# Optimization experiments

Measured on AMD Instinct MI355X. Metric: run time of the kernel, lower is better.

The kernel has to match this reference:

```python
import jax, jax.numpy as jnp
import numpy as np

K = 1048576          # number of shooting particles (k); x also has K points
LR = 0.25            # fixed-point gradient-descent learning rate
N_ITERS = 20         # nr_of_fixed_point_iterations
nl = jnp.tanh        # nonlinearity='tanh'


def _advect(z, t1, b1, t2, b2):
    # z: [n, 2, 1]; t*: [2,2]; b*: [2,1]. dot z = theta1 @ nl(theta2 @ z + b2) + b1
    return jnp.matmul(t1, nl(jnp.matmul(t2, z) + b2)) + b1


def _lagrangian(t1, b1, t2, b2, q, p, invK, invKb):
    eye = jnp.eye(2, dtype=t1.dtype)
    v1 = t1.reshape(-1)
    v2 = (t2 - eye).reshape(-1)
    kinetic = 0.5 * (v1 @ invK @ v1 + v2 @ invK @ v2
                     + b1[:, 0] @ invKb @ b1[:, 0] + b2[:, 0] @ invKb @ b2[:, 0])
    potential = jnp.mean(p * _advect(q, t1, b1, t2, b2))
    return kinetic - potential


def _run_fixed_point(q, p, t1, b1, t2, b2, invK, invKb):
    grad_fn = jax.grad(_lagrangian, argnums=(0, 1, 2, 3))
    def step(carry, _):
        t1, b1, t2, b2 = carry
        g1, gb1, g2, gb2 = grad_fn(t1, b1, t2, b2, q, p, invK, invKb)
        return (t1 - LR * g1, b1 - LR * gb1, t2 - LR * g2, b2 - LR * gb2), None
    carry, _ = jax.lax.scan(step, (t1, b1, t2, b2), None, length=N_ITERS)
    return carry


def setup_inputs() -> dict:
    key = jax.random.key(0)
    k1, k2, k3, k4, k5 = jax.random.split(key, 5)
    inp = jax.random.normal(k1, (3 * K, 1, 2), dtype=jnp.float32)
    return {
        "t": jnp.zeros((1,), dtype=jnp.float32),
        "inp": inp,
        "theta1_init": jax.random.normal(k2, (2, 2), dtype=jnp.float32),
        "bias1_init": jax.random.normal(k3, (2, 1), dtype=jnp.float32),
        "theta2_init": jax.random.normal(k4, (2, 2), dtype=jnp.float32),
        "bias2_init": jax.random.normal(k5, (2, 1), dtype=jnp.float32),
        "inv_Kbar": jnp.eye(4, dtype=jnp.float32),    # Kbar = I(d^2) -> inverse = I
        "inv_Kbar_b": jnp.eye(2, dtype=jnp.float32),  # Kbar_b = I(d) -> inverse = I
        "k": K,
    }


def reference(t, inp, theta1_init, bias1_init, theta2_init, bias2_init,
              inv_Kbar, inv_Kbar_b, k):
    qt, pt, xt = inp[:k], inp[k:2 * k], inp[2 * k:]
    q = jnp.swapaxes(qt, 1, 2)  # [k, 2, 1]
    p = jnp.swapaxes(pt, 1, 2)
    x = jnp.swapaxes(xt, 1, 2)

    def final_thetas(qv):
        return _run_fixed_point(qv, p, theta1_init, bias1_init,
                                theta2_init, bias2_init, inv_Kbar, inv_Kbar_b)

    t1, b1, t2, b2 = final_thetas(q)

    # dot_p = dL/dq of the final Lagrangian, including dependence of the
    # fixed-point thetas on q (torch uses create_graph=True throughout).
    def L_of_q(qv):
        ft1, fb1, ft2, fb2 = final_thetas(qv)
        return _lagrangian(ft1, fb1, ft2, fb2, qv, p, inv_Kbar, inv_Kbar_b)

    dot_p = jax.grad(L_of_q)(q)
    dot_x = _advect(x, t1, b1, t2, b2)
    dot_q = _advect(q, t1, b1, t2, b2)

    return jnp.concatenate([jnp.swapaxes(dot_q, 1, 2),
                            jnp.swapaxes(dot_p, 1, 2),
                            jnp.swapaxes(dot_x, 1, 2)], axis=0)
```

## Files before the change

kernel.cpp:

```cpp
#include <hip/hip_runtime.h>


#define LR 0.25f
#define NIT 20
#define TPB 512
#define NB  256
#define GUARD (1<<18)

typedef float v2f __attribute__((ext_vector_type(2)));
typedef unsigned long long u64;

__device__ __forceinline__ u64 ld64_ag(const u64* p){
    return __hip_atomic_load(p, __ATOMIC_RELAXED, __HIP_MEMORY_SCOPE_AGENT);
}
__device__ __forceinline__ void st64_ep(u64* p, float v, unsigned ep){
    u64 x = ((u64)ep << 32) | (u64)__float_as_uint(v);
    __hip_atomic_store(p, x, __ATOMIC_RELAXED, __HIP_MEMORY_SCOPE_AGENT);
}
__device__ __forceinline__ unsigned ep_of(u64 x){ return (unsigned)(x >> 32); }
__device__ __forceinline__ float    val_of(u64 x){ return __uint_as_float((unsigned)(x & 0xffffffffull)); }

__device__ __forceinline__ v2f tanh2(v2f x){
    v2f e;
    e.x = __expf(x.x + x.x);
    e.y = __expf(x.y + x.y);
    v2f d = e + 1.0f;
    v2f r;
    r.x = __builtin_amdgcn_rcpf(d.x);
    r.y = __builtin_amdgcn_rcpf(d.y);
    return 1.0f - (r + r);
}

#define DPP_ADD(x, ctrl) ((x) + __int_as_float(__builtin_amdgcn_update_dpp(0, __float_as_int(x), (ctrl), 0xF, 0xF, true)))
__device__ __forceinline__ float wave_sum64(float x){
    x = DPP_ADD(x, 0x111);
    x = DPP_ADD(x, 0x112);
    x = DPP_ADD(x, 0x114);
    x = DPP_ADD(x, 0x118);
    x = DPP_ADD(x, 0x142);
    x = DPP_ADD(x, 0x143);
    return x;
}

__device__ __forceinline__ void compute_grad(const float* s, const float* th,
                                             const float* ksym, const float* ksymb,
                                             float c, float* g){
    const float Ivec[4]={1.f,0.f,0.f,1.f};
    #pragma unroll
    for(int j=0;j<4;j++){
        float kv=0.f;
        #pragma unroll
        for(int m=0;m<4;m++) kv += ksym[j*4+m]*th[m];
        g[j] = kv - c*s[j];
    }
    #pragma unroll
    for(int i2=0;i2<2;i2++)
        g[4+i2] = ksymb[i2*2+0]*th[4] + ksymb[i2*2+1]*th[5] - c*s[4+i2];
    #pragma unroll
    for(int j=0;j<4;j++){
        float kv=0.f;
        #pragma unroll
        for(int m=0;m<4;m++) kv += ksym[j*4+m]*(th[6+m]-Ivec[m]);
        g[6+j] = kv - c*s[6+j];
    }
    #pragma unroll
    for(int i2=0;i2<2;i2++)
        g[10+i2] = ksymb[i2*2+0]*th[10] + ksymb[i2*2+1]*th[11] - c*s[10+i2];
}

__device__ __forceinline__ void accum_sample2(v2f Q0, v2f Q1, v2f P0, v2f P1,
    float t1_00,float t1_01,float t1_10,float t1_11,
    float t2_00,float t2_01,float t2_10,float t2_11,float b2_0,float b2_1,
    v2f (&acc)[36]){
    v2f u0 = t2_00*Q0 + t2_01*Q1 + b2_0;
    v2f u1 = t2_10*Q0 + t2_11*Q1 + b2_1;
    v2f h0 = tanh2(u0), h1 = tanh2(u1);
    v2f s0 = 1.0f - h0*h0, s1 = 1.0f - h1*h1;
    v2f a0 = t1_00*P0 + t1_10*P1;
    v2f a1 = t1_01*P0 + t1_11*P1;
    v2f w0 = a0*s0, w1 = a1*s1;
    v2f r0 = -2.0f*(a0*h0)*s0, r1 = -2.0f*(a1*h1)*s1;
    acc[0]+=P0*h0; acc[1]+=P0*h1; acc[2]+=P1*h0; acc[3]+=P1*h1;
    acc[4]+=P0;    acc[5]+=P1;
    acc[6]+=w0*Q0; acc[7]+=w0*Q1; acc[8]+=w1*Q0; acc[9]+=w1*Q1;
    acc[10]+=w0;   acc[11]+=w1;
    v2f ps00=P0*s0, ps01=P0*s1, ps10=P1*s0, ps11=P1*s1;
    acc[12]+=ps00*Q0; acc[13]+=ps00*Q1; acc[14]+=ps01*Q0; acc[15]+=ps01*Q1;
    acc[16]+=ps10*Q0; acc[17]+=ps10*Q1; acc[18]+=ps11*Q0; acc[19]+=ps11*Q1;
    acc[20]+=ps00; acc[21]+=ps01; acc[22]+=ps10; acc[23]+=ps11;
    v2f r0q0=r0*Q0, r1q0=r1*Q0;
    acc[24]+=r0q0*Q0; acc[25]+=r0q0*Q1; acc[26]+=r0*(Q1*Q1);
    acc[27]+=r1q0*Q0; acc[28]+=r1q0*Q1; acc[29]+=r1*(Q1*Q1);
    acc[30]+=r0q0; acc[31]+=r0*Q1; acc[32]+=r1q0; acc[33]+=r1*Q1;
    acc[34]+=r0; acc[35]+=r1;
}

__device__ __forceinline__ void bk_step2(v2f Q0, v2f Q1, v2f P0, v2f P1,
    float t1_00,float t1_01,float t1_10,float t1_11,
    float t2_00,float t2_01,float t2_10,float t2_11,float b2_0,float b2_1,
    float L1_00,float L1_01,float L1_10,float L1_11,
    float L2_00,float L2_01,float L2_10,float L2_11,float lb2_0,float lb2_1,
    v2f &B0, v2f &B1){
    v2f u0 = t2_00*Q0 + t2_01*Q1 + b2_0;
    v2f u1 = t2_10*Q0 + t2_11*Q1 + b2_1;
    v2f h0 = tanh2(u0), h1 = tanh2(u1);
    v2f s0 = 1.0f - h0*h0, s1 = 1.0f - h1*h1;
    v2f a0 = t1_00*P0 + t1_10*P1;
    v2f a1 = t1_01*P0 + t1_11*P1;
    v2f w0 = a0*s0, w1 = a1*s1;
    v2f r0 = -2.0f*(a0*h0)*s0, r1 = -2.0f*(a1*h1)*s1;
    v2f lp0 = L1_00*P0 + L1_10*P1;
    v2f lp1 = L1_01*P0 + L1_11*P1;
    v2f z0 = L2_00*Q0 + L2_01*Q1 + lb2_0;
    v2f z1 = L2_10*Q0 + L2_11*Q1 + lb2_1;
    v2f m0 = lp0*s0 + r0*z0;
    v2f m1 = lp1*s1 + r1*z1;
    B0 += t2_00*m0 + t2_10*m1 + L2_00*w0 + L2_10*w1;
    B1 += t2_01*m0 + t2_11*m1 + L2_01*w0 + L2_11*w1;
}

__global__ __launch_bounds__(TPB, 2) void k_all(
    const float4* __restrict__ q4, const float4* __restrict__ p4,
    const float4* __restrict__ x4, int nv4,
    const float* __restrict__ t1i, const float* __restrict__ b1i,
    const float* __restrict__ t2i, const float* __restrict__ b2i,
    const float* __restrict__ invK, const float* __restrict__ invKb,
    u64* __restrict__ part64,
    u64* __restrict__ tslot64,
    u64* __restrict__ pk64,
    float4* __restrict__ oq, float4* __restrict__ op, float4* __restrict__ ox,
    float c)
{
    const int tid  = threadIdx.x;
    const int bid  = blockIdx.x;
    const int NT   = gridDim.x * TPB;
    const int gtid = bid*TPB + tid;
    const int wave = tid >> 6, lane = tid & 63;

    __shared__ float ths[12];
    __shared__ float thetaAll[(NIT+1)*12];
    __shared__ float sAll[(NIT+1)*36];
    __shared__ float red[TPB/64][36];
    __shared__ float ks[16], ksb[4];
    __shared__ float4 pkS[NIT*5];
    float* pkSf = (float*)pkS;

    if(tid < 16) ks[tid]  = 0.5f*(invK[tid]  + invK[(tid&3)*4 + (tid>>2)]);
    if(tid < 4)  ksb[tid] = 0.5f*(invKb[tid] + invKb[(tid&1)*2 + (tid>>1)]);
    if(tid < 12){
        float v = (tid<4)? t1i[tid] : (tid<6)? b1i[tid-4]
                : (tid<10)? t2i[tid-6] : b2i[tid-10];
        ths[tid] = v;
        thetaAll[tid] = v;
    }
    __syncthreads();

    const bool fast = (nv4 == 4*NT);
    float4 qd[4], pd[4];
    if(fast){
        #pragma unroll
        for(int sl=0; sl<4; sl++){ qd[sl]=q4[gtid + sl*NT]; pd[sl]=p4[gtid + sl*NT]; }
    }

    for(int k=0; k<=NIT; k++){
        const float t1_00=ths[0], t1_01=ths[1], t1_10=ths[2], t1_11=ths[3];
        const float t2_00=ths[6], t2_01=ths[7], t2_10=ths[8], t2_11=ths[9];
        const float b2_0=ths[10], b2_1=ths[11];

        v2f acc[36];
        #pragma unroll
        for(int j=0;j<36;j++) acc[j] = (v2f){0.f, 0.f};

        if(fast){
            #pragma unroll
            for(int sl=0; sl<4; sl++){
                v2f Q0={qd[sl].x,qd[sl].z}, Q1={qd[sl].y,qd[sl].w};
                v2f P0={pd[sl].x,pd[sl].z}, P1={pd[sl].y,pd[sl].w};
                accum_sample2(Q0,Q1,P0,P1,
                    t1_00,t1_01,t1_10,t1_11,t2_00,t2_01,t2_10,t2_11,b2_0,b2_1,acc);
            }
        }else{
            for(int j = gtid; j < nv4; j += NT){
                float4 qq = q4[j], pp = p4[j];
                v2f Q0={qq.x,qq.z}, Q1={qq.y,qq.w};
                v2f P0={pp.x,pp.z}, P1={pp.y,pp.w};
                accum_sample2(Q0,Q1,P0,P1,
                    t1_00,t1_01,t1_10,t1_11,t2_00,t2_01,t2_10,t2_11,b2_0,b2_1,acc);
            }
        }

        float wres[36];
        #pragma unroll
        for(int j=0;j<36;j++) wres[j] = wave_sum64(acc[j].x + acc[j].y);
        if(lane == 63){
            #pragma unroll
            for(int j=0;j<36;j++) red[wave][j] = wres[j];
        }
        __syncthreads();
        if(tid < 36){
            float sum = 0.f;
            #pragma unroll
            for(int w=0; w<TPB/64; w++) sum += red[w][tid];
            st64_ep(part64 + tid*NB + bid, sum, (unsigned)(k+1));
        }

        if(bid == 0){
            const unsigned tgt = (unsigned)(k+1);
            const int r4i = (wave<4)? (wave+32) : (wave+24);
            const u64* R0 = part64 + (size_t)(wave     )*NB;
            const u64* R1 = part64 + (size_t)(wave +  8)*NB;
            const u64* R2 = part64 + (size_t)(wave + 16)*NB;
            const u64* R3 = part64 + (size_t)(wave + 24)*NB;
            const u64* R4 = part64 + (size_t)(r4i      )*NB;
            u64 a0,a1,a2,a3, b0,b1,b2,b3, c0,c1,c2,c3, d0,d1,d2,d3, e0,e1,e2,e3;
            int guard = 0;
            for(;;){
                a0=ld64_ag(R0+lane); a1=ld64_ag(R0+lane+64); a2=ld64_ag(R0+lane+128); a3=ld64_ag(R0+lane+192);
                b0=ld64_ag(R1+lane); b1=ld64_ag(R1+lane+64); b2=ld64_ag(R1+lane+128); b3=ld64_ag(R1+lane+192);
                c0=ld64_ag(R2+lane); c1=ld64_ag(R2+lane+64); c2=ld64_ag(R2+lane+128); c3=ld64_ag(R2+lane+192);
                d0=ld64_ag(R3+lane); d1=ld64_ag(R3+lane+64); d2=ld64_ag(R3+lane+128); d3=ld64_ag(R3+lane+192);
                e0=ld64_ag(R4+lane); e1=ld64_ag(R4+lane+64); e2=ld64_ag(R4+lane+128); e3=ld64_ag(R4+lane+192);
                bool ok = ep_of(a0)>=tgt && ep_of(a1)>=tgt && ep_of(a2)>=tgt && ep_of(a3)>=tgt
                       && ep_of(b0)>=tgt && ep_of(b1)>=tgt && ep_of(b2)>=tgt && ep_of(b3)>=tgt
                       && ep_of(c0)>=tgt && ep_of(c1)>=tgt && ep_of(c2)>=tgt && ep_of(c3)>=tgt
                       && ep_of(d0)>=tgt && ep_of(d1)>=tgt && ep_of(d2)>=tgt && ep_of(d3)>=tgt
                       && ep_of(e0)>=tgt && ep_of(e1)>=tgt && ep_of(e2)>=tgt && ep_of(e3)>=tgt;
                if(__all(ok)) break;
                __builtin_amdgcn_s_sleep(1);
                if(++guard > GUARD) break;
            }
            float s0 = wave_sum64(val_of(a0)+val_of(a1)+val_of(a2)+val_of(a3));
            float s1 = wave_sum64(val_of(b0)+val_of(b1)+val_of(b2)+val_of(b3));
            float s2 = wave_sum64(val_of(c0)+val_of(c1)+val_of(c2)+val_of(c3));
            float s3 = wave_sum64(val_of(d0)+val_of(d1)+val_of(d2)+val_of(d3));
            float s4 = wave_sum64(val_of(e0)+val_of(e1)+val_of(e2)+val_of(e3));
            if(lane == 63){
                sAll[k*36 + wave]      = s0;
                sAll[k*36 + wave + 8]  = s1;
                sAll[k*36 + wave + 16] = s2;
                sAll[k*36 + wave + 24] = s3;
                if(wave < 4) sAll[k*36 + wave + 32] = s4;
            }
            __syncthreads();
            if(tid == 0 && k < NIT){
                float g[12];
                compute_grad(sAll + k*36, thetaAll + k*12, ks, ksb, c, g);
                #pragma unroll
                for(int j=0;j<12;j++){
                    float t = thetaAll[k*12+j] - LR*g[j];
                    ths[j] = t;
                    thetaAll[(k+1)*12+j] = t;
                }
            }
            __syncthreads();
            if(k < NIT){
                for(int f = tid; f < NB*12; f += TPB)
                    st64_ep(tslot64 + f, ths[f % 12], (unsigned)(k+1));
            }
        }else if(k < NIT){
            if(wave == 0){
                const unsigned tgt = (unsigned)(k+1);
                const u64* sp = tslot64 + bid*12;
                const int idx = (lane < 12)? lane : 0;
                u64 v; int guard = 0;
                for(;;){
                    v = ld64_ag(sp + idx);
                    bool ok = (lane < 12)? (ep_of(v) >= tgt) : true;
                    if(__all(ok)) break;
                    __builtin_amdgcn_s_sleep(8);
                    if(++guard > GUARD) break;
                }
                if(lane < 12) ths[lane] = val_of(v);
            }
            __syncthreads();
        }
    }

    if(bid == 0){
        if(tid == 0){
            float lv[12];
            compute_grad(sAll + NIT*36, thetaAll + NIT*12, ks, ksb, c, lv);
            for(int k=NIT-1;k>=0;k--){
                const float* s = sAll + k*36;
                const float* T = thetaAll + k*12;
                float* P = (float*)&pkS[k*5];
                P[0]=T[0]; P[1]=T[1]; P[2]=T[2]; P[3]=T[3];
                P[4]=T[6]; P[5]=T[7]; P[6]=T[8]; P[7]=T[9];
                P[8]=T[10]; P[9]=T[11];
                P[10]=lv[0]; P[11]=lv[1]; P[12]=lv[2]; P[13]=lv[3];
                P[14]=lv[6]; P[15]=lv[7]; P[16]=lv[8]; P[17]=lv[9];
                P[18]=lv[10]; P[19]=lv[11];
                float H[12];
                for(int a=0;a<2;a++)for(int b=0;b<2;b++){
                    int j=a*2+b;
                    float data = s[12+a*4+b*2+0]*lv[6+b*2+0]
                               + s[12+a*4+b*2+1]*lv[6+b*2+1]
                               + s[20+a*2+b]*lv[10+b];
                    float kv=0.f;
                    for(int m=0;m<4;m++) kv += ks[j*4+m]*lv[m];
                    H[j]=kv - c*data;
                }
                H[4] = ksb[0]*lv[4] + ksb[1]*lv[5];
                H[5] = ksb[2]*lv[4] + ksb[3]*lv[5];
                for(int cc=0;cc<2;cc++)for(int d=0;d<2;d++){
                    int j=cc*2+d;
                    float term1 = lv[0+cc]*s[12+0*4+cc*2+d] + lv[2+cc]*s[12+1*4+cc*2+d];
                    float term2 = lv[6+cc*2+0]*s[24+cc*3+(0+d)] + lv[6+cc*2+1]*s[24+cc*3+(1+d)];
                    float term3 = lv[10+cc]*s[30+cc*2+d];
                    float kv=0.f;
                    for(int m=0;m<4;m++) kv += ks[j*4+m]*lv[6+m];
                    H[6+j]=kv - c*(term1+term2+term3);
                }
                for(int cc=0;cc<2;cc++){
                    float z1 = lv[0+cc]*s[20+0*2+cc] + lv[2+cc]*s[20+1*2+cc];
                    float z2 = lv[6+cc*2+0]*s[30+cc*2+0] + lv[6+cc*2+1]*s[30+cc*2+1];
                    float z3 = lv[10+cc]*s[34+cc];
                    float kv = ksb[cc*2+0]*lv[10] + ksb[cc*2+1]*lv[11];
                    H[10+cc]=kv - c*(z1+z2+z3);
                }
                for(int j=0;j<12;j++) lv[j] -= LR*H[j];
            }
        }
        __syncthreads();
        if(tid < NIT*20) st64_ep(pk64 + tid, pkSf[tid], (unsigned)(NIT+1));
    }else{
        if(tid < NIT*20){
            u64 v; int guard = 0;
            for(;;){
                v = ld64_ag(pk64 + tid);
                if(ep_of(v) >= (unsigned)(NIT+1)) break;
                __builtin_amdgcn_s_sleep(8);
                if(++guard > GUARD) break;
            }
            pkSf[tid] = val_of(v);
        }
        __syncthreads();
    }

    const float f1_00=ths[0], f1_01=ths[1], f1_10=ths[2], f1_11=ths[3];
    const float fb1_0=ths[4], fb1_1=ths[5];
    const float f2_00=ths[6], f2_01=ths[7], f2_10=ths[8], f2_11=ths[9];
    const float fb2_0=ths[10], fb2_1=ths[11];

    if(fast){
        v2f Q0r[4],Q1r[4],P0r[4],P1r[4],B0r[4],B1r[4];
        #pragma unroll
        for(int sl=0; sl<4; sl++){
            Q0r[sl]=(v2f){qd[sl].x,qd[sl].z}; Q1r[sl]=(v2f){qd[sl].y,qd[sl].w};
            P0r[sl]=(v2f){pd[sl].x,pd[sl].z}; P1r[sl]=(v2f){pd[sl].y,pd[sl].w};
            B0r[sl]=(v2f){0.f,0.f}; B1r[sl]=(v2f){0.f,0.f};
        }
        for(int k=0;k<NIT;k++){
            float4 P0=pkS[k*5+0], P1=pkS[k*5+1], P2=pkS[k*5+2], P3=pkS[k*5+3], P4v=pkS[k*5+4];
            float t1_00=P0.x,t1_01=P0.y,t1_10=P0.z,t1_11=P0.w;
            float t2_00=P1.x,t2_01=P1.y,t2_10=P1.z,t2_11=P1.w;
            float b2_0=P2.x,b2_1=P2.y;
            float L1_00=P2.z,L1_01=P2.w,L1_10=P3.x,L1_11=P3.y;
            float L2_00=P3.z,L2_01=P3.w,L2_10=P4v.x,L2_11=P4v.y,lb2_0=P4v.z,lb2_1=P4v.w;
            #pragma unroll
            for(int sl=0; sl<4; sl++)
                bk_step2(Q0r[sl],Q1r[sl],P0r[sl],P1r[sl],
                    t1_00,t1_01,t1_10,t1_11,t2_00,t2_01,t2_10,t2_11,b2_0,b2_1,
                    L1_00,L1_01,L1_10,L1_11,L2_00,L2_01,L2_10,L2_11,lb2_0,lb2_1,
                    B0r[sl],B1r[sl]);
        }
        #pragma unroll
        for(int sl=0; sl<4; sl++){
            int j = gtid + sl*NT;
            v2f Q0=Q0r[sl], Q1=Q1r[sl], P0=P0r[sl], P1=P1r[sl];
            v2f Bs0=B0r[sl], Bs1=B1r[sl];
            v2f u0 = f2_00*Q0 + f2_01*Q1 + fb2_0;
            v2f u1 = f2_10*Q0 + f2_11*Q1 + fb2_1;
            v2f h0 = tanh2(u0), h1 = tanh2(u1);
            v2f s0 = 1.0f - h0*h0, s1 = 1.0f - h1*h1;
            v2f a0 = f1_00*P0 + f1_10*P1;
            v2f a1 = f1_01*P0 + f1_11*P1;
            v2f w0 = a0*s0, w1 = a1*s1;
            v2f dq0 = f1_00*h0 + f1_01*h1 + fb1_0;
            v2f dq1 = f1_10*h0 + f1_11*h1 + fb1_1;
            v2f dp0 = c*(LR*Bs0 - (f2_00*w0 + f2_10*w1));
            v2f dp1 = c*(LR*Bs1 - (f2_01*w0 + f2_11*w1));
            oq[j] = make_float4(dq0.x, dq1.x, dq0.y, dq1.y);
            op[j] = make_float4(dp0.x, dp1.x, dp0.y, dp1.y);
            float4 xx = x4[j];
            v2f X0={xx.x,xx.z}, X1={xx.y,xx.w};
            v2f xu0 = f2_00*X0 + f2_01*X1 + fb2_0;
            v2f xu1 = f2_10*X0 + f2_11*X1 + fb2_1;
            v2f xh0 = tanh2(xu0), xh1 = tanh2(xu1);
            v2f xd0 = f1_00*xh0 + f1_01*xh1 + fb1_0;
            v2f xd1 = f1_10*xh0 + f1_11*xh1 + fb1_1;
            ox[j] = make_float4(xd0.x, xd1.x, xd0.y, xd1.y);
        }
    }else{
        for(int j = gtid; j < nv4; j += NT){
            float4 qq=q4[j], pp=p4[j];
            v2f Q0={qq.x,qq.z}, Q1={qq.y,qq.w};
            v2f P0={pp.x,pp.z}, P1={pp.y,pp.w};
            v2f Bs0={0.f,0.f}, Bs1={0.f,0.f};
            for(int k=0;k<NIT;k++){
                float4 P0v=pkS[k*5+0], P1v=pkS[k*5+1], P2v=pkS[k*5+2], P3v=pkS[k*5+3], P4v=pkS[k*5+4];
                bk_step2(Q0,Q1,P0,P1,
                    P0v.x,P0v.y,P0v.z,P0v.w, P1v.x,P1v.y,P1v.z,P1v.w, P2v.x,P2v.y,
                    P2v.z,P2v.w,P3v.x,P3v.y, P3v.z,P3v.w,P4v.x,P4v.y,P4v.z,P4v.w,
                    Bs0,Bs1);
            }
            v2f u0 = f2_00*Q0 + f2_01*Q1 + fb2_0;
            v2f u1 = f2_10*Q0 + f2_11*Q1 + fb2_1;
            v2f h0 = tanh2(u0), h1 = tanh2(u1);
            v2f s0 = 1.0f - h0*h0, s1 = 1.0f - h1*h1;
            v2f a0 = f1_00*P0 + f1_10*P1;
            v2f a1 = f1_01*P0 + f1_11*P1;
            v2f w0 = a0*s0, w1 = a1*s1;
            v2f dq0 = f1_00*h0 + f1_01*h1 + fb1_0;
            v2f dq1 = f1_10*h0 + f1_11*h1 + fb1_1;
            v2f dp0 = c*(LR*Bs0 - (f2_00*w0 + f2_10*w1));
            v2f dp1 = c*(LR*Bs1 - (f2_01*w0 + f2_11*w1));
            oq[j] = make_float4(dq0.x, dq1.x, dq0.y, dq1.y);
            op[j] = make_float4(dp0.x, dp1.x, dp0.y, dp1.y);
            float4 xx = x4[j];
            v2f X0={xx.x,xx.z}, X1={xx.y,xx.w};
            v2f xu0 = f2_00*X0 + f2_01*X1 + fb2_0;
            v2f xu1 = f2_10*X0 + f2_11*X1 + fb2_1;
            v2f xh0 = tanh2(xu0), xh1 = tanh2(xu1);
            v2f xd0 = f1_00*xh0 + f1_01*xh1 + fb1_0;
            v2f xd1 = f1_10*xh0 + f1_11*xh1 + fb1_1;
            ox[j] = make_float4(xd0.x, xd1.x, xd0.y, xd1.y);
        }
    }
}

extern "C" void kernel_launch(void* const* d_in, const int* in_sizes, int n_in,
                              void* d_out, int out_size, void* d_ws, size_t ws_size,
                              hipStream_t stream) {
    const float* inp = (const float*)d_in[1];
    const int K = in_sizes[1]/6;
    int nv4 = K >> 1;

    const float4* q4 = (const float4*)inp;
    const float4* p4 = (const float4*)(inp + 2*(size_t)K);
    const float4* x4 = (const float4*)(inp + 4*(size_t)K);

    u64* part64  = (u64*)d_ws;
    u64* tslot64 = part64 + 36*NB;
    u64* pk64    = tslot64 + NB*12;
    float c = 1.0f/(2.0f*(float)K);

    const float* t1i = (const float*)d_in[2];
    const float* b1i = (const float*)d_in[3];
    const float* t2i = (const float*)d_in[4];
    const float* b2i = (const float*)d_in[5];
    const float* invK = (const float*)d_in[6];
    const float* invKb= (const float*)d_in[7];

    float* out = (float*)d_out;
    float4* oq = (float4*)out;
    float4* op = (float4*)(out + 2*(size_t)K);
    float4* ox = (float4*)(out + 4*(size_t)K);

    size_t zb = (size_t)(36*NB + NB*12 + 400)*sizeof(u64);
    hipMemsetAsync(d_ws, 0, zb, stream);
    k_all<<<dim3(NB), dim3(TPB), 0, stream>>>(q4, p4, x4, nv4,
                                              t1i, b1i, t2i, b2i, invK, invKb,
                                              part64, tslot64, pk64, oq, op, ox, c);
}
```

Before: 261.6 us.

## Overlap dot_q/dot_x output with wait for backward coefficients

Moves the dot_q and dot_x computation and stores, which need only the final thetas, ahead of the wait for block 0's serial backward pass that publishes the per-iteration coefficients. The other blocks now do useful memory work while block 0 computes the adjoint recursion. Only then do they poll the packed coefficients, with a single wave loading them in batches. The polling sleep intervals are shortened and the guard raised. Q/P are re-extracted from loaded registers rather than kept in separate arrays.

```diff
diff --git a/kernel.cpp b/kernel.cpp
--- a/kernel.cpp
+++ b/kernel.cpp
@@ -5,7 +5,7 @@
 #define NIT 20
 #define TPB 512
 #define NB  256
-#define GUARD (1<<18)
+#define GUARD (1<<20)
 
 typedef float v2f __attribute__((ext_vector_type(2)));
 typedef unsigned long long u64;
@@ -267,7 +267,7 @@
                     v = ld64_ag(sp + idx);
                     bool ok = (lane < 12)? (ep_of(v) >= tgt) : true;
                     if(__all(ok)) break;
-                    __builtin_amdgcn_s_sleep(8);
+                    __builtin_amdgcn_s_sleep(2);
                     if(++guard > GUARD) break;
                 }
                 if(lane < 12) ths[lane] = val_of(v);
@@ -323,18 +323,6 @@
         }
         __syncthreads();
         if(tid < NIT*20) st64_ep(pk64 + tid, pkSf[tid], (unsigned)(NIT+1));
-    }else{
-        if(tid < NIT*20){
-            u64 v; int guard = 0;
-            for(;;){
-                v = ld64_ag(pk64 + tid);
-                if(ep_of(v) >= (unsigned)(NIT+1)) break;
-                __builtin_amdgcn_s_sleep(8);
-                if(++guard > GUARD) break;
-            }
-            pkSf[tid] = val_of(v);
-        }
-        __syncthreads();
     }
 
     const float f1_00=ths[0], f1_01=ths[1], f1_10=ths[2], f1_11=ths[3];
@@ -343,13 +331,54 @@
     const float fb2_0=ths[10], fb2_1=ths[11];
 
     if(fast){
-        v2f Q0r[4],Q1r[4],P0r[4],P1r[4],B0r[4],B1r[4];
         #pragma unroll
         for(int sl=0; sl<4; sl++){
-            Q0r[sl]=(v2f){qd[sl].x,qd[sl].z}; Q1r[sl]=(v2f){qd[sl].y,qd[sl].w};
-            P0r[sl]=(v2f){pd[sl].x,pd[sl].z}; P1r[sl]=(v2f){pd[sl].y,pd[sl].w};
-            B0r[sl]=(v2f){0.f,0.f}; B1r[sl]=(v2f){0.f,0.f};
-        }
+            int j = gtid + sl*NT;
+            v2f Q0={qd[sl].x,qd[sl].z}, Q1={qd[sl].y,qd[sl].w};
+            v2f u0 = f2_00*Q0 + f2_01*Q1 + fb2_0;
+            v2f u1 = f2_10*Q0 + f2_11*Q1 + fb2_1;
+            v2f h0 = tanh2(u0), h1 = tanh2(u1);
+            v2f dq0 = f1_00*h0 + f1_01*h1 + fb1_0;
+            v2f dq1 = f1_10*h0 + f1_11*h1 + fb1_1;
+            oq[j] = make_float4(dq0.x, dq1.x, dq0.y, dq1.y);
+            float4 xx = x4[j];
+            v2f X0={xx.x,xx.z}, X1={xx.y,xx.w};
+            v2f xu0 = f2_00*X0 + f2_01*X1 + fb2_0;
+            v2f xu1 = f2_10*X0 + f2_11*X1 + fb2_1;
+            v2f xh0 = tanh2(xu0), xh1 = tanh2(xu1);
+            v2f xd0 = f1_00*xh0 + f1_01*xh1 + fb1_0;
+            v2f xd1 = f1_10*xh0 + f1_11*xh1 + fb1_1;
+            ox[j] = make_float4(xd0.x, xd1.x, xd0.y, xd1.y);
+        }
+        if(bid != 0){
+            if(wave == 0){
+                const unsigned tgt = (unsigned)(NIT+1);
+                u64 v[7]; int guard = 0;
+                for(;;){
+                    bool ok = true;
+                    #pragma unroll
+                    for(int i=0;i<7;i++){
+                        int idx = lane + i*64;
+                        if(idx < NIT*20){
+                            v[i] = ld64_ag(pk64 + idx);
+                            ok = ok && (ep_of(v[i]) >= tgt);
+                        }
+                    }
+                    if(__all(ok)) break;
+                    __builtin_amdgcn_s_sleep(4);
+                    if(++guard > GUARD) break;
+                }
+                #pragma unroll
+                for(int i=0;i<7;i++){
+                    int idx = lane + i*64;
+                    if(idx < NIT*20) pkSf[idx] = val_of(v[i]);
+                }
+            }
+            __syncthreads();
+        }
+        v2f B0r[4],B1r[4];
+        #pragma unroll
+        for(int sl=0; sl<4; sl++){ B0r[sl]=(v2f){0.f,0.f}; B1r[sl]=(v2f){0.f,0.f}; }
         for(int k=0;k<NIT;k++){
             float4 P0=pkS[k*5+0], P1=pkS[k*5+1], P2=pkS[k*5+2], P3=pkS[k*5+3], P4v=pkS[k*5+4];
             float t1_00=P0.x,t1_01=P0.y,t1_10=P0.z,t1_11=P0.w;
@@ -358,17 +387,20 @@
             float L1_00=P2.z,L1_01=P2.w,L1_10=P3.x,L1_11=P3.y;
             float L2_00=P3.z,L2_01=P3.w,L2_10=P4v.x,L2_11=P4v.y,lb2_0=P4v.z,lb2_1=P4v.w;
             #pragma unroll
-            for(int sl=0; sl<4; sl++)
-                bk_step2(Q0r[sl],Q1r[sl],P0r[sl],P1r[sl],
+            for(int sl=0; sl<4; sl++){
+                v2f Q0={qd[sl].x,qd[sl].z}, Q1={qd[sl].y,qd[sl].w};
+                v2f P0s={pd[sl].x,pd[sl].z}, P1s={pd[sl].y,pd[sl].w};
+                bk_step2(Q0,Q1,P0s,P1s,
                     t1_00,t1_01,t1_10,t1_11,t2_00,t2_01,t2_10,t2_11,b2_0,b2_1,
                     L1_00,L1_01,L1_10,L1_11,L2_00,L2_01,L2_10,L2_11,lb2_0,lb2_1,
                     B0r[sl],B1r[sl]);
+            }
         }
         #pragma unroll
         for(int sl=0; sl<4; sl++){
             int j = gtid + sl*NT;
-            v2f Q0=Q0r[sl], Q1=Q1r[sl], P0=P0r[sl], P1=P1r[sl];
-            v2f Bs0=B0r[sl], Bs1=B1r[sl];
+            v2f Q0={qd[sl].x,qd[sl].z}, Q1={qd[sl].y,qd[sl].w};
+            v2f P0={pd[sl].x,pd[sl].z}, P1={pd[sl].y,pd[sl].w};
             v2f u0 = f2_00*Q0 + f2_01*Q1 + fb2_0;
             v2f u1 = f2_10*Q0 + f2_11*Q1 + fb2_1;
             v2f h0 = tanh2(u0), h1 = tanh2(u1);
@@ -376,12 +408,20 @@
             v2f a0 = f1_00*P0 + f1_10*P1;
             v2f a1 = f1_01*P0 + f1_11*P1;
             v2f w0 = a0*s0, w1 = a1*s1;
+            v2f dp0 = c*(LR*B0r[sl] - (f2_00*w0 + f2_10*w1));
+            v2f dp1 = c*(LR*B1r[sl] - (f2_01*w0 + f2_11*w1));
+            op[j] = make_float4(dp0.x, dp1.x, dp0.y, dp1.y);
+        }
+    }else{
+        for(int j = gtid; j < nv4; j += NT){
+            float4 qq=q4[j];
+            v2f Q0={qq.x,qq.z}, Q1={qq.y,qq.w};
+            v2f u0 = f2_00*Q0 + f2_01*Q1 + fb2_0;
+            v2f u1 = f2_10*Q0 + f2_11*Q1 + fb2_1;
+            v2f h0 = tanh2(u0), h1 = tanh2(u1);
             v2f dq0 = f1_00*h0 + f1_01*h1 + fb1_0;
             v2f dq1 = f1_10*h0 + f1_11*h1 + fb1_1;
-            v2f dp0 = c*(LR*Bs0 - (f2_00*w0 + f2_10*w1));
-            v2f dp1 = c*(LR*Bs1 - (f2_01*w0 + f2_11*w1));
             oq[j] = make_float4(dq0.x, dq1.x, dq0.y, dq1.y);
-            op[j] = make_float4(dp0.x, dp1.x, dp0.y, dp1.y);
             float4 xx = x4[j];
             v2f X0={xx.x,xx.z}, X1={xx.y,xx.w};
             v2f xu0 = f2_00*X0 + f2_01*X1 + fb2_0;
@@ -391,7 +431,32 @@
             v2f xd1 = f1_10*xh0 + f1_11*xh1 + fb1_1;
             ox[j] = make_float4(xd0.x, xd1.x, xd0.y, xd1.y);
         }
-    }else{
+        if(bid != 0){
+            if(wave == 0){
+                const unsigned tgt = (unsigned)(NIT+1);
+                u64 v[7]; int guard = 0;
+                for(;;){
+                    bool ok = true;
+                    #pragma unroll
+                    for(int i=0;i<7;i++){
+                        int idx = lane + i*64;
+                        if(idx < NIT*20){
+                            v[i] = ld64_ag(pk64 + idx);
+                            ok = ok && (ep_of(v[i]) >= tgt);
+                        }
+                    }
+                    if(__all(ok)) break;
+                    __builtin_amdgcn_s_sleep(4);
+                    if(++guard > GUARD) break;
+                }
+                #pragma unroll
+                for(int i=0;i<7;i++){
+                    int idx = lane + i*64;
+                    if(idx < NIT*20) pkSf[idx] = val_of(v[i]);
+                }
+            }
+            __syncthreads();
+        }
         for(int j = gtid; j < nv4; j += NT){
             float4 qq=q4[j], pp=p4[j];
             v2f Q0={qq.x,qq.z}, Q1={qq.y,qq.w};
@@ -411,20 +476,9 @@
             v2f a0 = f1_00*P0 + f1_10*P1;
             v2f a1 = f1_01*P0 + f1_11*P1;
             v2f w0 = a0*s0, w1 = a1*s1;
-            v2f dq0 = f1_00*h0 + f1_01*h1 + fb1_0;
-            v2f dq1 = f1_10*h0 + f1_11*h1 + fb1_1;
             v2f dp0 = c*(LR*Bs0 - (f2_00*w0 + f2_10*w1));
             v2f dp1 = c*(LR*Bs1 - (f2_01*w0 + f2_11*w1));
-            oq[j] = make_float4(dq0.x, dq1.x, dq0.y, dq1.y);
             op[j] = make_float4(dp0.x, dp1.x, dp0.y, dp1.y);
-            float4 xx = x4[j];
-            v2f X0={xx.x,xx.z}, X1={xx.y,xx.w};
-            v2f xu0 = f2_00*X0 + f2_01*X1 + fb2_0;
-            v2f xu1 = f2_10*X0 + f2_11*X1 + fb2_1;
-            v2f xh0 = tanh2(xu0), xh1 = tanh2(xu1);
-            v2f xd0 = f1_00*xh0 + f1_01*xh1 + fb1_0;
-            v2f xd1 = f1_10*xh0 + f1_11*xh1 + fb1_1;
-            ox[j] = make_float4(xd0.x, xd1.x, xd0.y, xd1.y);
         }
     }
 }
```

Result: faster. 254.7 us (-2.6%).
